# Kernel tuning notes

Measured on AMD Instinct MI355X. Metric: run time of the kernel, lower is better.

The kernel has to match this reference:

```python
import jax, jax.numpy as jnp
import numpy as np

B, S, E, H, V, L = 64, 128, 512, 1024, 32000, 1


def setup_inputs() -> dict:
    key = jax.random.key(0)
    ks = jax.random.split(key, 12)
    def rn(k, shape, scale=0.02):
        return jax.random.normal(k, shape, dtype=jnp.float32) * scale
    return dict(
        emb=rn(ks[0], (B, E), 1.0),
        hidden=rn(ks[1], (L, B, H), 1.0),
        encoder_outputs=rn(ks[2], (S, B, H), 1.0),
        z=rn(ks[3], (B, H), 1.0),
        # Attn('concat'): W_a [H, 2H], bias, scoring vector v [H]
        Wa=rn(ks[4], (H, 2 * H)), ba=jnp.zeros((H,), jnp.float32),
        v=rn(ks[5], (H,)),
        # CustomGRUCell: input/hidden/context/latent-z to 3*H gate projections
        Wx=rn(ks[6], (3 * H, E)), bx=jnp.zeros((3 * H,), jnp.float32),
        Wh=rn(ks[7], (3 * H, H)), bh=jnp.zeros((3 * H,), jnp.float32),
        Wc=rn(ks[8], (3 * H, H)), bc=jnp.zeros((3 * H,), jnp.float32),
        Wz=rn(ks[9], (3 * H, H)), bz=jnp.zeros((3 * H,), jnp.float32),
        # rnn2out: Linear(H, V)
        Wout=rn(ks[10], (V, H)), bout=jnp.zeros((V,), jnp.float32),
    )


def reference(emb, hidden, encoder_outputs, z, Wa, ba, v,
              Wx, bx, Wh, bh, Wc, bc, Wz, bz, Wout, bout):
    h_last = hidden[-1]                                              # [B,H]
    # Bahdanau 'concat' attention: score = v . tanh(Wa @ [h; enc] + ba)
    hS = jnp.broadcast_to(h_last[None], encoder_outputs.shape)       # [S,B,H]
    energy = jnp.tanh(jnp.concatenate([hS, encoder_outputs], axis=-1) @ Wa.T + ba)  # [S,B,H]
    scores = jnp.einsum('sbh,h->bs', energy, v)                      # [B,S]
    attn_weights = jax.nn.softmax(scores, axis=-1)[:, None, :]       # [B,1,S]
    enc_bt = jnp.transpose(encoder_outputs, (1, 0, 2))               # [B,S,H]
    context = jnp.einsum('bos,bsh->bh', attn_weights, enc_bt)        # [B,H]
    # Custom GRU cell: gates get extra context and latent-z additive terms
    gx = emb @ Wx.T + bx                                             # [B,3H]
    gh = h_last @ Wh.T + bh
    gc = context @ Wc.T + bc
    gz = z @ Wz.T + bz
    xr, xu, xn = jnp.split(gx + gc + gz, 3, axis=-1)
    hr, hu, hn = jnp.split(gh, 3, axis=-1)
    r = jax.nn.sigmoid(xr + hr)                                      # reset gate
    u = jax.nn.sigmoid(xu + hu)                                      # update gate
    n = jnp.tanh(xn + r * hn)                                        # candidate
    h_new = (1.0 - u) * n + u * h_last                               # [B,H]
    out = h_new @ Wout.T + bout                                      # [B,V] logits
    return out, h_new[None], attn_weights
```

## Files before the change

kernel.cpp:

```cpp
#include <hip/hip_runtime.h>
#include <hip/hip_bf16.h>
#include <math.h>

#define B_  64
#define S_  128
#define E_  512
#define H_  1024
#define V_  32000
#define H3_ 3072
#define NT_ 16

typedef __attribute__((ext_vector_type(8))) short bf16x8;
typedef __attribute__((ext_vector_type(4))) float f32x4;

__device__ __forceinline__ unsigned short f2b(float f) {
    unsigned int u = __builtin_bit_cast(unsigned int, f);
    u = (u + 0x7fffu + ((u >> 16) & 1u)) >> 16;
    return (unsigned short)u;
}

__global__ void cast_bf16(const float* __restrict__ in, unsigned short* __restrict__ out) {
    const size_t i8 = ((size_t)blockIdx.x * 256 + threadIdx.x) * 8;
    float4 a = *(const float4*)&in[i8];
    float4 b = *(const float4*)&in[i8 + 4];
    unsigned short o[8] = { f2b(a.x), f2b(a.y), f2b(a.z), f2b(a.w),
                            f2b(b.x), f2b(b.y), f2b(b.z), f2b(b.w) };
    *(uint4*)&out[i8] = *(uint4*)o;
}

__global__ void cast_wa2(const float* __restrict__ Wa, unsigned short* __restrict__ out) {
    const int id = blockIdx.x * 256 + threadIdx.x;
    const int n = id >> 7;
    const int kk = (id & 127) * 8;
    const float* src = &Wa[(size_t)n * (2 * H_) + H_ + kk];
    float4 a = *(const float4*)src;
    float4 b = *(const float4*)(src + 4);
    unsigned short o[8] = { f2b(a.x), f2b(a.y), f2b(a.z), f2b(a.w),
                            f2b(b.x), f2b(b.y), f2b(b.z), f2b(b.w) };
    *(uint4*)&out[(size_t)n * H_ + kk] = *(uint4*)o;
}

__device__ __forceinline__ void tile_acc(const float* __restrict__ A, int lda,
                                         const float* __restrict__ Wrow0, int ldw,
                                         int kspan, int t, float c[4][4],
                                         float (*As)[64], float (*Ws)[64]) {
    const int tx = t & 15, ty = t >> 4;
    const int lm = t >> 2;
    const int lk = (t & 3) * 4;
    for (int k0 = 0; k0 < kspan; k0 += 16) {
        float4 av = *(const float4*)&A[lm * lda + k0 + lk];
        float4 wv = *(const float4*)&Wrow0[(size_t)lm * ldw + k0 + lk];
        As[lk + 0][lm] = av.x; As[lk + 1][lm] = av.y;
        As[lk + 2][lm] = av.z; As[lk + 3][lm] = av.w;
        Ws[lk + 0][lm] = wv.x; Ws[lk + 1][lm] = wv.y;
        Ws[lk + 2][lm] = wv.z; Ws[lk + 3][lm] = wv.w;
        __syncthreads();
        #pragma unroll
        for (int k = 0; k < 16; ++k) {
            float4 a = *(const float4*)&As[k][ty * 4];
            float4 w = *(const float4*)&Ws[k][tx * 4];
            c[0][0] += a.x * w.x; c[0][1] += a.x * w.y; c[0][2] += a.x * w.z; c[0][3] += a.x * w.w;
            c[1][0] += a.y * w.x; c[1][1] += a.y * w.y; c[1][2] += a.y * w.z; c[1][3] += a.y * w.w;
            c[2][0] += a.z * w.x; c[2][1] += a.z * w.y; c[2][2] += a.z * w.z; c[2][3] += a.z * w.w;
            c[3][0] += a.w * w.x; c[3][1] += a.w * w.y; c[3][2] += a.w * w.z; c[3][3] += a.w * w.w;
        }
        __syncthreads();
    }
}

__global__ void gemm_nt(const float* __restrict__ A, const float* __restrict__ W,
                        const float* __restrict__ bias, float* __restrict__ C,
                        int N, int K) {
    __shared__ float As[16][64];
    __shared__ float Ws[16][64];
    const int n0 = blockIdx.x * 64;
    const int t  = threadIdx.x;
    const int tx = t & 15, ty = t >> 4;
    float c[4][4];
    #pragma unroll
    for (int i = 0; i < 4; ++i)
        #pragma unroll
        for (int j = 0; j < 4; ++j) c[i][j] = 0.f;
    tile_acc(A, K, &W[(size_t)n0 * K], K, K, t, c, As, Ws);
    #pragma unroll
    for (int i = 0; i < 4; ++i) {
        const int m = ty * 4 + i;
        #pragma unroll
        for (int j = 0; j < 4; ++j) {
            const int n = n0 + tx * 4 + j;
            C[m * N + n] = c[i][j] + bias[n];
        }
    }
}

__global__ __launch_bounds__(256) void wout_mfma(
    const unsigned short* __restrict__ Ab, const float* __restrict__ W,
    const float* __restrict__ bias, float* __restrict__ C) {
    __shared__ unsigned short As[64 * 64];
    __shared__ unsigned short Bs[64 * 64];
    const int n0 = blockIdx.x * 64;
    const int t = threadIdx.x;
    const int lane = t & 63, w = t >> 6;
    const int wr = w >> 1, wc = w & 1;

    f32x4 acc[2][2];
    #pragma unroll
    for (int i = 0; i < 2; ++i)
        #pragma unroll
        for (int j = 0; j < 2; ++j) acc[i][j] = (f32x4){0.f, 0.f, 0.f, 0.f};

    for (int k0 = 0; k0 < H_; k0 += 64) {
        #pragma unroll
        for (int r = 0; r < 2; ++r) {
            const int c = r * 256 + t;
            const int row = c >> 3, slot = c & 7;
            const int sw = slot ^ (row & 7);
            uint4 da = *(const uint4*)&Ab[(size_t)row * H_ + k0 + slot * 8];
            *(uint4*)((char*)As + row * 128 + sw * 16) = da;
        }
        #pragma unroll
        for (int r = 0; r < 4; ++r) {
            const int c = r * 256 + t;
            const int row = c >> 4, q4 = c & 15;
            const float4 wv = *(const float4*)&W[(size_t)(n0 + row) * H_ + k0 + q4 * 4];
            uint2 pk;
            pk.x = (unsigned int)f2b(wv.x) | ((unsigned int)f2b(wv.y) << 16);
            pk.y = (unsigned int)f2b(wv.z) | ((unsigned int)f2b(wv.w) << 16);
            const int slot = q4 >> 1, half = q4 & 1;
            const int sw = slot ^ (row & 7);
            *(uint2*)((char*)Bs + row * 128 + sw * 16 + half * 8) = pk;
        }
        __syncthreads();
        #pragma unroll
        for (int kk = 0; kk < 2; ++kk) {
            bf16x8 a[2], b[2];
            #pragma unroll
            for (int i = 0; i < 2; ++i) {
                const int row = wr * 32 + i * 16 + (lane & 15);
                const int sw = (kk * 4 + (lane >> 4)) ^ (row & 7);
                a[i] = *(const bf16x8*)((const char*)As + row * 128 + sw * 16);
            }
            #pragma unroll
            for (int j = 0; j < 2; ++j) {
                const int row = wc * 32 + j * 16 + (lane & 15);
                const int sw = (kk * 4 + (lane >> 4)) ^ (row & 7);
                b[j] = *(const bf16x8*)((const char*)Bs + row * 128 + sw * 16);
            }
            #pragma unroll
            for (int i = 0; i < 2; ++i)
                #pragma unroll
                for (int j = 0; j < 2; ++j)
                    acc[i][j] = __builtin_amdgcn_mfma_f32_16x16x32_bf16(a[i], b[j], acc[i][j], 0, 0, 0);
        }
        __syncthreads();
    }

    #pragma unroll
    for (int i = 0; i < 2; ++i)
        #pragma unroll
        for (int j = 0; j < 2; ++j) {
            const int n = n0 + wc * 32 + j * 16 + (lane & 15);
            const float bn = bias[n];
            #pragma unroll
            for (int q = 0; q < 4; ++q) {
                const int m = wr * 32 + i * 16 + (lane >> 4) * 4 + q;
                C[(size_t)m * V_ + n] = acc[i][j][q] + bn;
            }
        }
}

__global__ void hproj_splitk(const float* __restrict__ h, const float* __restrict__ Wa,
                             float* __restrict__ hpp) {
    __shared__ float As[16][64];
    __shared__ float Ws[16][64];
    const int n0 = blockIdx.x * 64;
    const int kb = blockIdx.y * 128;
    const int t  = threadIdx.x;
    const int tx = t & 15, ty = t >> 4;
    float c[4][4];
    #pragma unroll
    for (int i = 0; i < 4; ++i)
        #pragma unroll
        for (int j = 0; j < 4; ++j) c[i][j] = 0.f;
    tile_acc(&h[kb], H_, &Wa[(size_t)n0 * (2 * H_) + kb], 2 * H_, 128, t, c, As, Ws);
    float* dst = hpp + (size_t)blockIdx.y * B_ * H_;
    #pragma unroll
    for (int i = 0; i < 4; ++i) {
        const int m = ty * 4 + i;
        #pragma unroll
        for (int j = 0; j < 4; ++j)
            dst[m * H_ + n0 + tx * 4 + j] = c[i][j];
    }
}

__global__ void reduce_hproj(const float* __restrict__ hpp, const float* __restrict__ ba,
                             float* __restrict__ hproj) {
    const int idx = blockIdx.x * 256 + threadIdx.x;
    const int hh = idx & 1023;
    float s = ba[hh];
    #pragma unroll
    for (int c = 0; c < 8; ++c) s += hpp[(size_t)c * B_ * H_ + idx];
    hproj[idx] = s;
}

__global__ void gates_splitk(const float* __restrict__ emb, const float* __restrict__ z,
                             const float* __restrict__ ctx, const float* __restrict__ h,
                             const float* __restrict__ Wx, const float* __restrict__ Wz,
                             const float* __restrict__ Wc, const float* __restrict__ Wh,
                             float* __restrict__ P) {
    __shared__ float As[16][64];
    __shared__ float Ws[16][64];
    const int n0 = blockIdx.x * 64;
    const int yc = blockIdx.y;
    const int t  = threadIdx.x;
    const int tx = t & 15, ty = t >> 4;

    const float* A; const float* W; int lda, kb;
    if (yc == 0)      { A = emb; W = Wx; lda = E_; kb = 0; }
    else if (yc <= 2) { A = z;   W = Wz; lda = H_; kb = (yc - 1) * 512; }
    else if (yc <= 4) { A = ctx; W = Wc; lda = H_; kb = (yc - 3) * 512; }
    else              { A = h;   W = Wh; lda = H_; kb = (yc - 5) * 512; }

    float c[4][4];
    #pragma unroll
    for (int i = 0; i < 4; ++i)
        #pragma unroll
        for (int j = 0; j < 4; ++j) c[i][j] = 0.f;
    tile_acc(&A[kb], lda, &W[(size_t)n0 * lda + kb], lda, 512, t, c, As, Ws);
    float* dst = P + (size_t)yc * B_ * H3_;
    #pragma unroll
    for (int i = 0; i < 4; ++i) {
        const int m = ty * 4 + i;
        #pragma unroll
        for (int j = 0; j < 4; ++j)
            dst[m * H3_ + n0 + tx * 4 + j] = c[i][j];
    }
}

__global__ __launch_bounds__(256) void energy_mfma(
    const unsigned short* __restrict__ Ab, const unsigned short* __restrict__ Bb,
    const float* __restrict__ hproj, const float* __restrict__ v,
    float* __restrict__ partials) {
    __shared__ unsigned short As[128 * 32];
    __shared__ unsigned short Bs[128 * 32];
    const int nb = blockIdx.x;
    const int mb = blockIdx.y;
    const int m0 = mb * 128, n0 = nb * 128;
    const int t = threadIdx.x;
    const int lane = t & 63, w = t >> 6;
    const int wr = w >> 1, wc = w & 1;

    f32x4 acc[4][4];
    #pragma unroll
    for (int i = 0; i < 4; ++i)
        #pragma unroll
        for (int j = 0; j < 4; ++j) acc[i][j] = (f32x4){0.f, 0.f, 0.f, 0.f};

    for (int k0 = 0; k0 < H_; k0 += 32) {
        #pragma unroll
        for (int r = 0; r < 2; ++r) {
            const int c = r * 256 + t;
            const int row = c >> 2, slot = c & 3;
            const int sw = slot ^ ((row >> 1) & 3);
            uint4 da = *(const uint4*)&Ab[(size_t)(m0 + row) * H_ + k0 + slot * 8];
            *(uint4*)((char*)As + row * 64 + sw * 16) = da;
            uint4 db = *(const uint4*)&Bb[(size_t)(n0 + row) * H_ + k0 + slot * 8];
            *(uint4*)((char*)Bs + row * 64 + sw * 16) = db;
        }
        __syncthreads();
        bf16x8 a[4], b[4];
        #pragma unroll
        for (int i = 0; i < 4; ++i) {
            const int row = wr * 64 + i * 16 + (lane & 15);
            const int sw = (lane >> 4) ^ ((row >> 1) & 3);
            a[i] = *(const bf16x8*)((const char*)As + row * 64 + sw * 16);
        }
        #pragma unroll
        for (int j = 0; j < 4; ++j) {
            const int row = wc * 64 + j * 16 + (lane & 15);
            const int sw = (lane >> 4) ^ ((row >> 1) & 3);
            b[j] = *(const bf16x8*)((const char*)Bs + row * 64 + sw * 16);
        }
        #pragma unroll
        for (int i = 0; i < 4; ++i)
            #pragma unroll
            for (int j = 0; j < 4; ++j)
                acc[i][j] = __builtin_amdgcn_mfma_f32_16x16x32_bf16(a[i], b[j], acc[i][j], 0, 0, 0);
        __syncthreads();
    }

    float vj[4];
    #pragma unroll
    for (int j = 0; j < 4; ++j) vj[j] = v[n0 + wc * 64 + j * 16 + (lane & 15)];

    const int s = mb * 2 + wr;
    #pragma unroll
    for (int i = 0; i < 4; ++i) {
        #pragma unroll
        for (int q = 0; q < 4; ++q) {
            const int b = i * 16 + (lane >> 4) * 4 + q;
            float sum = 0.f;
            #pragma unroll
            for (int j = 0; j < 4; ++j) {
                const int n = n0 + wc * 64 + j * 16 + (lane & 15);
                sum += vj[j] * tanhf(acc[i][j][q] + hproj[b * H_ + n]);
            }
            sum += __shfl_xor(sum, 1);
            sum += __shfl_xor(sum, 2);
            sum += __shfl_xor(sum, 4);
            sum += __shfl_xor(sum, 8);
            if ((lane & 15) == 0)
                partials[((size_t)b * S_ + s) * NT_ + nb * 2 + wc] = sum;
        }
    }
}

__global__ void energy_scores(const float* __restrict__ enc, const float* __restrict__ Wa,
                              const float* __restrict__ hproj, const float* __restrict__ v,
                              float* __restrict__ partials) {
    __shared__ float As[16][64];
    __shared__ float Ws[16][64];
    __shared__ float red[64][16];
    const int nt = blockIdx.x;
    const int s  = blockIdx.y;
    const int n0 = nt * 64;
    const float* Arow = enc + (size_t)s * (B_ * H_);
    const int t  = threadIdx.x;
    const int tx = t & 15, ty = t >> 4;
    float c[4][4];
    #pragma unroll
    for (int i = 0; i < 4; ++i)
        #pragma unroll
        for (int j = 0; j < 4; ++j) c[i][j] = 0.f;
    tile_acc(Arow, H_, &Wa[(size_t)n0 * (2 * H_) + H_], 2 * H_, H_, t, c, As, Ws);
    #pragma unroll
    for (int i = 0; i < 4; ++i) {
        const int b = ty * 4 + i;
        float part = 0.f;
        #pragma unroll
        for (int j = 0; j < 4; ++j) {
            const int h = n0 + tx * 4 + j;
            part += v[h] * tanhf(c[i][j] + hproj[b * H_ + h]);
        }
        red[b][tx] = part;
    }
    __syncthreads();
    if (t < 64) {
        float sum = 0.f;
        #pragma unroll
        for (int x = 0; x < 16; ++x) sum += red[t][x];
        partials[((size_t)t * S_ + s) * NT_ + nt] = sum;
    }
}

__global__ void softmax_attn(const float* __restrict__ partials, float* __restrict__ attn_out) {
    __shared__ float red[128];
    const int b = blockIdx.x;
    const int s = threadIdx.x;
    float sc = 0.f;
    #pragma unroll
    for (int nt = 0; nt < NT_; ++nt) sc += partials[((size_t)b * S_ + s) * NT_ + nt];
    red[s] = sc; __syncthreads();
    for (int o = 64; o > 0; o >>= 1) {
        if (s < o) red[s] = fmaxf(red[s], red[s + o]);
        __syncthreads();
    }
    const float mx = red[0]; __syncthreads();
    const float e = expf(sc - mx);
    red[s] = e; __syncthreads();
    for (int o = 64; o > 0; o >>= 1) {
        if (s < o) red[s] += red[s + o];
        __syncthreads();
    }
    attn_out[b * S_ + s] = e / red[0];
}

__global__ void context_k(const float* __restrict__ attn, const float* __restrict__ enc,
                          float* __restrict__ ctx) {
    __shared__ float aw[S_];
    const int b = blockIdx.y;
    const int h = blockIdx.x * 256 + threadIdx.x;
    if (threadIdx.x < S_) aw[threadIdx.x] = attn[b * S_ + threadIdx.x];
    __syncthreads();
    float acc = 0.f;
    for (int s = 0; s < S_; ++s)
        acc += aw[s] * enc[((size_t)s * B_ + b) * H_ + h];
    ctx[b * H_ + h] = acc;
}

__global__ void gru_k(const float* __restrict__ P, const float* __restrict__ hlast,
                      const float* __restrict__ bx, const float* __restrict__ bz,
                      const float* __restrict__ bc, const float* __restrict__ bh,
                      float* __restrict__ hnew) {
    const int idx = blockIdx.x * 256 + threadIdx.x;
    const int b = idx >> 10, h = idx & 1023;
    float x[3], hg[3];
    #pragma unroll
    for (int g = 0; g < 3; ++g) {
        const int col = g * H_ + h;
        float sx = bx[col] + bz[col] + bc[col];
        #pragma unroll
        for (int c = 0; c < 5; ++c) sx += P[((size_t)c * B_ + b) * H3_ + col];
        float sh = bh[col];
        #pragma unroll
        for (int c = 5; c < 7; ++c) sh += P[((size_t)c * B_ + b) * H3_ + col];
        x[g] = sx; hg[g] = sh;
    }
    const float r = 1.f / (1.f + expf(-(x[0] + hg[0])));
    const float u = 1.f / (1.f + expf(-(x[1] + hg[1])));
    const float n = tanhf(x[2] + r * hg[2]);
    hnew[idx] = (1.f - u) * n + u * hlast[idx];
}

extern "C" void kernel_launch(void* const* d_in, const int* in_sizes, int n_in,
                              void* d_out, int out_size, void* d_ws, size_t ws_size,
                              hipStream_t stream) {
    const float* emb   = (const float*)d_in[0];
    const float* hid   = (const float*)d_in[1];
    const float* enc   = (const float*)d_in[2];
    const float* z     = (const float*)d_in[3];
    const float* Wa    = (const float*)d_in[4];
    const float* ba    = (const float*)d_in[5];
    const float* v     = (const float*)d_in[6];
    const float* Wx    = (const float*)d_in[7];
    const float* bx    = (const float*)d_in[8];
    const float* Wh    = (const float*)d_in[9];
    const float* bh    = (const float*)d_in[10];
    const float* Wc    = (const float*)d_in[11];
    const float* bc    = (const float*)d_in[12];
    const float* Wz    = (const float*)d_in[13];
    const float* bz    = (const float*)d_in[14];
    const float* Wout  = (const float*)d_in[15];
    const float* bout  = (const float*)d_in[16];

    float* out  = (float*)d_out;
    float* hnew = out + (size_t)B_ * V_;
    float* attn = hnew + (size_t)B_ * H_;

    float* hproj = (float*)d_ws;
    float* spart = hproj + (size_t)B_ * H_;
    float* ctx   = spart + (size_t)B_ * S_ * NT_;
    float* uni   = ctx + (size_t)B_ * H_;
    unsigned short* encb = (unsigned short*)uni;
    unsigned short* wa2b = encb + (size_t)S_ * B_ * H_;
    float* hpp   = uni;
    float* P     = uni;
    unsigned short* hnewb = (unsigned short*)(P + (size_t)7 * B_ * H3_);
    const size_t need = (size_t)((char*)(wa2b + (size_t)H_ * H_) - (char*)d_ws);

    const float* hlast = hid;
    dim3 blk(256);

    hproj_splitk<<<dim3(H_ / 64, 8), blk, 0, stream>>>(hlast, Wa, hpp);
    reduce_hproj<<<dim3((B_ * H_) / 256), blk, 0, stream>>>(hpp, ba, hproj);

    const bool fast = (ws_size >= need);
    if (fast) {
        cast_bf16<<<dim3((S_ * B_ * H_) / (256 * 8)), blk, 0, stream>>>(enc, encb);
        cast_wa2<<<dim3((H_ * H_) / (256 * 8)), blk, 0, stream>>>(Wa, wa2b);
        energy_mfma<<<dim3(H_ / 128, (S_ * B_) / 128), blk, 0, stream>>>(encb, wa2b, hproj, v, spart);
    } else {
        energy_scores<<<dim3(NT_, S_), blk, 0, stream>>>(enc, Wa, hproj, v, spart);
    }

    softmax_attn<<<dim3(B_), dim3(S_), 0, stream>>>(spart, attn);
    context_k<<<dim3(H_ / 256, B_), blk, 0, stream>>>(attn, enc, ctx);

    gates_splitk<<<dim3(H3_ / 64, 7), blk, 0, stream>>>(emb, z, ctx, hlast,
                                                        Wx, Wz, Wc, Wh, P);
    gru_k<<<dim3((B_ * H_) / 256), blk, 0, stream>>>(P, hlast, bx, bz, bc, bh, hnew);

    if (fast) {
        cast_bf16<<<dim3((B_ * H_) / (256 * 8)), blk, 0, stream>>>(hnew, hnewb);
        wout_mfma<<<dim3(V_ / 64), blk, 0, stream>>>(hnewb, Wout, bout, out);
    } else {
        gemm_nt<<<dim3(V_ / 64), blk, 0, stream>>>(hnew, Wout, bout, out, V_, H_);
    }
}
```

Before: 147.6 us.

## Fuse prologue casts with hproj, merge softmax into context, cast hnew in GRU

The enc and Wa bf16 casts and the hproj split-K GEMM are merged into one heterogeneous prologue launch, so hpp gets its own workspace region instead of aliasing the cast buffers. Softmax is folded into the context kernel, with each block recomputing its batch row's softmax, and the GRU kernel writes the bf16 copy of h_new directly. This removes four launches and lets the small hproj GEMM overlap the bandwidth-bound casts. The cost is redundant softmax work across the four H-blocks per batch and a larger workspace requirement.

```diff
diff --git a/kernel.cpp b/kernel.cpp
--- a/kernel.cpp
+++ b/kernel.cpp
@@ -17,27 +17,6 @@
     unsigned int u = __builtin_bit_cast(unsigned int, f);
     u = (u + 0x7fffu + ((u >> 16) & 1u)) >> 16;
     return (unsigned short)u;
-}
-
-__global__ void cast_bf16(const float* __restrict__ in, unsigned short* __restrict__ out) {
-    const size_t i8 = ((size_t)blockIdx.x * 256 + threadIdx.x) * 8;
-    float4 a = *(const float4*)&in[i8];
-    float4 b = *(const float4*)&in[i8 + 4];
-    unsigned short o[8] = { f2b(a.x), f2b(a.y), f2b(a.z), f2b(a.w),
-                            f2b(b.x), f2b(b.y), f2b(b.z), f2b(b.w) };
-    *(uint4*)&out[i8] = *(uint4*)o;
-}
-
-__global__ void cast_wa2(const float* __restrict__ Wa, unsigned short* __restrict__ out) {
-    const int id = blockIdx.x * 256 + threadIdx.x;
-    const int n = id >> 7;
-    const int kk = (id & 127) * 8;
-    const float* src = &Wa[(size_t)n * (2 * H_) + H_ + kk];
-    float4 a = *(const float4*)src;
-    float4 b = *(const float4*)(src + 4);
-    unsigned short o[8] = { f2b(a.x), f2b(a.y), f2b(a.z), f2b(a.w),
-                            f2b(b.x), f2b(b.y), f2b(b.z), f2b(b.w) };
-    *(uint4*)&out[(size_t)n * H_ + kk] = *(uint4*)o;
 }
 
 __device__ __forceinline__ void tile_acc(const float* __restrict__ A, int lda,
@@ -68,129 +47,64 @@
     }
 }
 
-__global__ void gemm_nt(const float* __restrict__ A, const float* __restrict__ W,
-                        const float* __restrict__ bias, float* __restrict__ C,
-                        int N, int K) {
+__device__ __forceinline__ void hproj_body(int bx, int by, const float* __restrict__ h,
+                                           const float* __restrict__ Wa, float* __restrict__ hpp,
+                                           int t, float (*As)[64], float (*Ws)[64]) {
+    const int n0 = bx * 64;
+    const int kb = by * 128;
+    const int tx = t & 15, ty = t >> 4;
+    float c[4][4];
+    #pragma unroll
+    for (int i = 0; i < 4; ++i)
+        #pragma unroll
+        for (int j = 0; j < 4; ++j) c[i][j] = 0.f;
+    tile_acc(&h[kb], H_, &Wa[(size_t)n0 * (2 * H_) + kb], 2 * H_, 128, t, c, As, Ws);
+    float* dst = hpp + (size_t)by * B_ * H_;
+    #pragma unroll
+    for (int i = 0; i < 4; ++i) {
+        const int m = ty * 4 + i;
+        #pragma unroll
+        for (int j = 0; j < 4; ++j)
+            dst[m * H_ + n0 + tx * 4 + j] = c[i][j];
+    }
+}
+
+__global__ __launch_bounds__(256) void prologue(
+    const float* __restrict__ enc, const float* __restrict__ Wa,
+    const float* __restrict__ h, unsigned short* __restrict__ encb,
+    unsigned short* __restrict__ wa2b, float* __restrict__ hpp) {
     __shared__ float As[16][64];
     __shared__ float Ws[16][64];
-    const int n0 = blockIdx.x * 64;
-    const int t  = threadIdx.x;
-    const int tx = t & 15, ty = t >> 4;
-    float c[4][4];
-    #pragma unroll
-    for (int i = 0; i < 4; ++i)
-        #pragma unroll
-        for (int j = 0; j < 4; ++j) c[i][j] = 0.f;
-    tile_acc(A, K, &W[(size_t)n0 * K], K, K, t, c, As, Ws);
-    #pragma unroll
-    for (int i = 0; i < 4; ++i) {
-        const int m = ty * 4 + i;
-        #pragma unroll
-        for (int j = 0; j < 4; ++j) {
-            const int n = n0 + tx * 4 + j;
-            C[m * N + n] = c[i][j] + bias[n];
-        }
-    }
-}
-
-__global__ __launch_bounds__(256) void wout_mfma(
-    const unsigned short* __restrict__ Ab, const float* __restrict__ W,
-    const float* __restrict__ bias, float* __restrict__ C) {
-    __shared__ unsigned short As[64 * 64];
-    __shared__ unsigned short Bs[64 * 64];
-    const int n0 = blockIdx.x * 64;
+    const int bid = blockIdx.x;
     const int t = threadIdx.x;
-    const int lane = t & 63, w = t >> 6;
-    const int wr = w >> 1, wc = w & 1;
-
-    f32x4 acc[2][2];
-    #pragma unroll
-    for (int i = 0; i < 2; ++i)
-        #pragma unroll
-        for (int j = 0; j < 2; ++j) acc[i][j] = (f32x4){0.f, 0.f, 0.f, 0.f};
-
-    for (int k0 = 0; k0 < H_; k0 += 64) {
-        #pragma unroll
-        for (int r = 0; r < 2; ++r) {
-            const int c = r * 256 + t;
-            const int row = c >> 3, slot = c & 7;
-            const int sw = slot ^ (row & 7);
-            uint4 da = *(const uint4*)&Ab[(size_t)row * H_ + k0 + slot * 8];
-            *(uint4*)((char*)As + row * 128 + sw * 16) = da;
-        }
-        #pragma unroll
-        for (int r = 0; r < 4; ++r) {
-            const int c = r * 256 + t;
-            const int row = c >> 4, q4 = c & 15;
-            const float4 wv = *(const float4*)&W[(size_t)(n0 + row) * H_ + k0 + q4 * 4];
-            uint2 pk;
-            pk.x = (unsigned int)f2b(wv.x) | ((unsigned int)f2b(wv.y) << 16);
-            pk.y = (unsigned int)f2b(wv.z) | ((unsigned int)f2b(wv.w) << 16);
-            const int slot = q4 >> 1, half = q4 & 1;
-            const int sw = slot ^ (row & 7);
-            *(uint2*)((char*)Bs + row * 128 + sw * 16 + half * 8) = pk;
-        }
-        __syncthreads();
-        #pragma unroll
-        for (int kk = 0; kk < 2; ++kk) {
-            bf16x8 a[2], b[2];
-            #pragma unroll
-            for (int i = 0; i < 2; ++i) {
-                const int row = wr * 32 + i * 16 + (lane & 15);
-                const int sw = (kk * 4 + (lane >> 4)) ^ (row & 7);
-                a[i] = *(const bf16x8*)((const char*)As + row * 128 + sw * 16);
-            }
-            #pragma unroll
-            for (int j = 0; j < 2; ++j) {
-                const int row = wc * 32 + j * 16 + (lane & 15);
-                const int sw = (kk * 4 + (lane >> 4)) ^ (row & 7);
-                b[j] = *(const bf16x8*)((const char*)Bs + row * 128 + sw * 16);
-            }
-            #pragma unroll
-            for (int i = 0; i < 2; ++i)
-                #pragma unroll
-                for (int j = 0; j < 2; ++j)
-                    acc[i][j] = __builtin_amdgcn_mfma_f32_16x16x32_bf16(a[i], b[j], acc[i][j], 0, 0, 0);
-        }
-        __syncthreads();
-    }
-
-    #pragma unroll
-    for (int i = 0; i < 2; ++i)
-        #pragma unroll
-        for (int j = 0; j < 2; ++j) {
-            const int n = n0 + wc * 32 + j * 16 + (lane & 15);
-            const float bn = bias[n];
-            #pragma unroll
-            for (int q = 0; q < 4; ++q) {
-                const int m = wr * 32 + i * 16 + (lane >> 4) * 4 + q;
-                C[(size_t)m * V_ + n] = acc[i][j][q] + bn;
-            }
-        }
+    if (bid < 4096) {
+        const size_t i8 = ((size_t)bid * 256 + t) * 8;
+        float4 a = *(const float4*)&enc[i8];
+        float4 b = *(const float4*)&enc[i8 + 4];
+        unsigned short o[8] = { f2b(a.x), f2b(a.y), f2b(a.z), f2b(a.w),
+                                f2b(b.x), f2b(b.y), f2b(b.z), f2b(b.w) };
+        *(uint4*)&encb[i8] = *(uint4*)o;
+    } else if (bid < 4608) {
+        const int id = (bid - 4096) * 256 + t;
+        const int n = id >> 7;
+        const int kk = (id & 127) * 8;
+        const float* src = &Wa[(size_t)n * (2 * H_) + H_ + kk];
+        float4 a = *(const float4*)src;
+        float4 b = *(const float4*)(src + 4);
+        unsigned short o[8] = { f2b(a.x), f2b(a.y), f2b(a.z), f2b(a.w),
+                                f2b(b.x), f2b(b.y), f2b(b.z), f2b(b.w) };
+        *(uint4*)&wa2b[(size_t)n * H_ + kk] = *(uint4*)o;
+    } else {
+        const int id = bid - 4608;
+        hproj_body(id & 15, id >> 4, h, Wa, hpp, t, As, Ws);
+    }
 }
 
 __global__ void hproj_splitk(const float* __restrict__ h, const float* __restrict__ Wa,
                              float* __restrict__ hpp) {
     __shared__ float As[16][64];
     __shared__ float Ws[16][64];
-    const int n0 = blockIdx.x * 64;
-    const int kb = blockIdx.y * 128;
-    const int t  = threadIdx.x;
-    const int tx = t & 15, ty = t >> 4;
-    float c[4][4];
-    #pragma unroll
-    for (int i = 0; i < 4; ++i)
-        #pragma unroll
-        for (int j = 0; j < 4; ++j) c[i][j] = 0.f;
-    tile_acc(&h[kb], H_, &Wa[(size_t)n0 * (2 * H_) + kb], 2 * H_, 128, t, c, As, Ws);
-    float* dst = hpp + (size_t)blockIdx.y * B_ * H_;
-    #pragma unroll
-    for (int i = 0; i < 4; ++i) {
-        const int m = ty * 4 + i;
-        #pragma unroll
-        for (int j = 0; j < 4; ++j)
-            dst[m * H_ + n0 + tx * 4 + j] = c[i][j];
-    }
+    hproj_body(blockIdx.x, blockIdx.y, h, Wa, hpp, threadIdx.x, As, Ws);
 }
 
 __global__ void reduce_hproj(const float* __restrict__ hpp, const float* __restrict__ ba,
@@ -201,40 +115,6 @@
     #pragma unroll
     for (int c = 0; c < 8; ++c) s += hpp[(size_t)c * B_ * H_ + idx];
     hproj[idx] = s;
-}
-
-__global__ void gates_splitk(const float* __restrict__ emb, const float* __restrict__ z,
-                             const float* __restrict__ ctx, const float* __restrict__ h,
-                             const float* __restrict__ Wx, const float* __restrict__ Wz,
-                             const float* __restrict__ Wc, const float* __restrict__ Wh,
-                             float* __restrict__ P) {
-    __shared__ float As[16][64];
-    __shared__ float Ws[16][64];
-    const int n0 = blockIdx.x * 64;
-    const int yc = blockIdx.y;
-    const int t  = threadIdx.x;
-    const int tx = t & 15, ty = t >> 4;
-
-    const float* A; const float* W; int lda, kb;
-    if (yc == 0)      { A = emb; W = Wx; lda = E_; kb = 0; }
-    else if (yc <= 2) { A = z;   W = Wz; lda = H_; kb = (yc - 1) * 512; }
-    else if (yc <= 4) { A = ctx; W = Wc; lda = H_; kb = (yc - 3) * 512; }
-    else              { A = h;   W = Wh; lda = H_; kb = (yc - 5) * 512; }
-
-    float c[4][4];
-    #pragma unroll
-    for (int i = 0; i < 4; ++i)
-        #pragma unroll
-        for (int j = 0; j < 4; ++j) c[i][j] = 0.f;
-    tile_acc(&A[kb], lda, &W[(size_t)n0 * lda + kb], lda, 512, t, c, As, Ws);
-    float* dst = P + (size_t)yc * B_ * H3_;
-    #pragma unroll
-    for (int i = 0; i < 4; ++i) {
-        const int m = ty * 4 + i;
-        #pragma unroll
-        for (int j = 0; j < 4; ++j)
-            dst[m * H3_ + n0 + tx * 4 + j] = c[i][j];
-    }
 }
 
 __global__ __launch_bounds__(256) void energy_mfma(
@@ -353,45 +233,84 @@
     }
 }
 
-__global__ void softmax_attn(const float* __restrict__ partials, float* __restrict__ attn_out) {
+__global__ __launch_bounds__(256) void softmax_ctx(
+    const float* __restrict__ spart, const float* __restrict__ enc,
+    float* __restrict__ attn, float* __restrict__ ctx) {
     __shared__ float red[128];
-    const int b = blockIdx.x;
-    const int s = threadIdx.x;
-    float sc = 0.f;
-    #pragma unroll
-    for (int nt = 0; nt < NT_; ++nt) sc += partials[((size_t)b * S_ + s) * NT_ + nt];
-    red[s] = sc; __syncthreads();
+    __shared__ float aw[128];
+    const int b = blockIdx.y;
+    const int t = threadIdx.x;
+    if (t < 128) {
+        float sc = 0.f;
+        #pragma unroll
+        for (int nt = 0; nt < NT_; ++nt) sc += spart[((size_t)b * S_ + t) * NT_ + nt];
+        aw[t] = sc;
+        red[t] = sc;
+    }
+    __syncthreads();
     for (int o = 64; o > 0; o >>= 1) {
-        if (s < o) red[s] = fmaxf(red[s], red[s + o]);
-        __syncthreads();
-    }
-    const float mx = red[0]; __syncthreads();
-    const float e = expf(sc - mx);
-    red[s] = e; __syncthreads();
+        if (t < o) red[t] = fmaxf(red[t], red[t + o]);
+        __syncthreads();
+    }
+    const float mx = red[0];
+    __syncthreads();
+    if (t < 128) { aw[t] = expf(aw[t] - mx); red[t] = aw[t]; }
+    __syncthreads();
     for (int o = 64; o > 0; o >>= 1) {
-        if (s < o) red[s] += red[s + o];
-        __syncthreads();
-    }
-    attn_out[b * S_ + s] = e / red[0];
-}
-
-__global__ void context_k(const float* __restrict__ attn, const float* __restrict__ enc,
-                          float* __restrict__ ctx) {
-    __shared__ float aw[S_];
-    const int b = blockIdx.y;
-    const int h = blockIdx.x * 256 + threadIdx.x;
-    if (threadIdx.x < S_) aw[threadIdx.x] = attn[b * S_ + threadIdx.x];
+        if (t < o) red[t] += red[t + o];
+        __syncthreads();
+    }
+    const float inv = 1.f / red[0];
+    if (t < 128) {
+        aw[t] *= inv;
+        if (blockIdx.x == 0) attn[b * S_ + t] = aw[t];
+    }
     __syncthreads();
+    const int h = blockIdx.x * 256 + t;
     float acc = 0.f;
     for (int s = 0; s < S_; ++s)
         acc += aw[s] * enc[((size_t)s * B_ + b) * H_ + h];
     ctx[b * H_ + h] = acc;
 }
 
+__global__ void gates_splitk(const float* __restrict__ emb, const float* __restrict__ z,
+                             const float* __restrict__ ctx, const float* __restrict__ h,
+                             const float* __restrict__ Wx, const float* __restrict__ Wz,
+                             const float* __restrict__ Wc, const float* __restrict__ Wh,
+                             float* __restrict__ P) {
+    __shared__ float As[16][64];
+    __shared__ float Ws[16][64];
+    const int n0 = blockIdx.x * 64;
+    const int yc = blockIdx.y;
+    const int t  = threadIdx.x;
+    const int tx = t & 15, ty = t >> 4;
+
+    const float* A; const float* W; int lda, kb;
+    if (yc == 0)      { A = emb; W = Wx; lda = E_; kb = 0; }
+    else if (yc <= 2) { A = z;   W = Wz; lda = H_; kb = (yc - 1) * 512; }
+    else if (yc <= 4) { A = ctx; W = Wc; lda = H_; kb = (yc - 3) * 512; }
+    else              { A = h;   W = Wh; lda = H_; kb = (yc - 5) * 512; }
+
+    float c[4][4];
+    #pragma unroll
+    for (int i = 0; i < 4; ++i)
+        #pragma unroll
+        for (int j = 0; j < 4; ++j) c[i][j] = 0.f;
+    tile_acc(&A[kb], lda, &W[(size_t)n0 * lda + kb], lda, 512, t, c, As, Ws);
+    float* dst = P + (size_t)yc * B_ * H3_;
+    #pragma unroll
+    for (int i = 0; i < 4; ++i) {
+        const int m = ty * 4 + i;
+        #pragma unroll
+        for (int j = 0; j < 4; ++j)
+            dst[m * H3_ + n0 + tx * 4 + j] = c[i][j];
+    }
+}
+
 __global__ void gru_k(const float* __restrict__ P, const float* __restrict__ hlast,
                       const float* __restrict__ bx, const float* __restrict__ bz,
                       const float* __restrict__ bc, const float* __restrict__ bh,
-                      float* __restrict__ hnew) {
+                      float* __restrict__ hnew, unsigned short* __restrict__ hnewb) {
     const int idx = blockIdx.x * 256 + threadIdx.x;
     const int b = idx >> 10, h = idx & 1023;
     float x[3], hg[3];
@@ -409,7 +328,110 @@
     const float r = 1.f / (1.f + expf(-(x[0] + hg[0])));
     const float u = 1.f / (1.f + expf(-(x[1] + hg[1])));
     const float n = tanhf(x[2] + r * hg[2]);
-    hnew[idx] = (1.f - u) * n + u * hlast[idx];
+    const float val = (1.f - u) * n + u * hlast[idx];
+    hnew[idx] = val;
+    if (hnewb) hnewb[idx] = f2b(val);
+}
+
+__global__ __launch_bounds__(256) void wout_mfma(
+    const unsigned short* __restrict__ Ab, const float* __restrict__ W,
+    const float* __restrict__ bias, float* __restrict__ C) {
+    __shared__ unsigned short As[64 * 64];
+    __shared__ unsigned short Bs[64 * 64];
+    const int n0 = blockIdx.x * 64;
+    const int t = threadIdx.x;
+    const int lane = t & 63, w = t >> 6;
+    const int wr = w >> 1, wc = w & 1;
+
+    f32x4 acc[2][2];
+    #pragma unroll
+    for (int i = 0; i < 2; ++i)
+        #pragma unroll
+        for (int j = 0; j < 2; ++j) acc[i][j] = (f32x4){0.f, 0.f, 0.f, 0.f};
+
+    for (int k0 = 0; k0 < H_; k0 += 64) {
+        #pragma unroll
+        for (int r = 0; r < 2; ++r) {
+            const int c = r * 256 + t;
+            const int row = c >> 3, slot = c & 7;
+            const int sw = slot ^ (row & 7);
+            uint4 da = *(const uint4*)&Ab[(size_t)row * H_ + k0 + slot * 8];
+            *(uint4*)((char*)As + row * 128 + sw * 16) = da;
+        }
+        #pragma unroll
+        for (int r = 0; r < 4; ++r) {
+            const int c = r * 256 + t;
+            const int row = c >> 4, q4 = c & 15;
+            const float4 wv = *(const float4*)&W[(size_t)(n0 + row) * H_ + k0 + q4 * 4];
+            uint2 pk;
+            pk.x = (unsigned int)f2b(wv.x) | ((unsigned int)f2b(wv.y) << 16);
+            pk.y = (unsigned int)f2b(wv.z) | ((unsigned int)f2b(wv.w) << 16);
+            const int slot = q4 >> 1, half = q4 & 1;
+            const int sw = slot ^ (row & 7);
+            *(uint2*)((char*)Bs + row * 128 + sw * 16 + half * 8) = pk;
+        }
+        __syncthreads();
+        #pragma unroll
+        for (int kk = 0; kk < 2; ++kk) {
+            bf16x8 a[2], b[2];
+            #pragma unroll
+            for (int i = 0; i < 2; ++i) {
+                const int row = wr * 32 + i * 16 + (lane & 15);
+                const int sw = (kk * 4 + (lane >> 4)) ^ (row & 7);
+                a[i] = *(const bf16x8*)((const char*)As + row * 128 + sw * 16);
+            }
+            #pragma unroll
+            for (int j = 0; j < 2; ++j) {
+                const int row = wc * 32 + j * 16 + (lane & 15);
+                const int sw = (kk * 4 + (lane >> 4)) ^ (row & 7);
+                b[j] = *(const bf16x8*)((const char*)Bs + row * 128 + sw * 16);
+            }
+            #pragma unroll
+            for (int i = 0; i < 2; ++i)
+                #pragma unroll
+                for (int j = 0; j < 2; ++j)
+                    acc[i][j] = __builtin_amdgcn_mfma_f32_16x16x32_bf16(a[i], b[j], acc[i][j], 0, 0, 0);
+        }
+        __syncthreads();
+    }
+
+    #pragma unroll
+    for (int i = 0; i < 2; ++i)
+        #pragma unroll
+        for (int j = 0; j < 2; ++j) {
+            const int n = n0 + wc * 32 + j * 16 + (lane & 15);
+            const float bn = bias[n];
+            #pragma unroll
+            for (int q = 0; q < 4; ++q) {
+                const int m = wr * 32 + i * 16 + (lane >> 4) * 4 + q;
+                C[(size_t)m * V_ + n] = acc[i][j][q] + bn;
+            }
+        }
+}
+
+__global__ void gemm_nt(const float* __restrict__ A, const float* __restrict__ W,
+                        const float* __restrict__ bias, float* __restrict__ C,
+                        int N, int K) {
+    __shared__ float As[16][64];
+    __shared__ float Ws[16][64];
+    const int n0 = blockIdx.x * 64;
+    const int t  = threadIdx.x;
+    const int tx = t & 15, ty = t >> 4;
+    float c[4][4];
+    #pragma unroll
+    for (int i = 0; i < 4; ++i)
+        #pragma unroll
+        for (int j = 0; j < 4; ++j) c[i][j] = 0.f;
+    tile_acc(A, K, &W[(size_t)n0 * K], K, K, t, c, As, Ws);
+    #pragma unroll
+    for (int i = 0; i < 4; ++i) {
+        const int m = ty * 4 + i;
+        #pragma unroll
+        for (int j = 0; j < 4; ++j) {
+            const int n = n0 + tx * 4 + j;
+            C[m * N + n] = c[i][j] + bias[n];
+        }
+    }
 }
 
 extern "C" void kernel_launch(void* const* d_in, const int* in_sizes, int n_in,
@@ -440,38 +462,36 @@
     float* hproj = (float*)d_ws;
     float* spart = hproj + (size_t)B_ * H_;
     float* ctx   = spart + (size_t)B_ * S_ * NT_;
-    float* uni   = ctx + (size_t)B_ * H_;
+    float* hpp   = ctx + (size_t)B_ * H_;
+    float* uni   = hpp + (size_t)8 * B_ * H_;
     unsigned short* encb = (unsigned short*)uni;
     unsigned short* wa2b = encb + (size_t)S_ * B_ * H_;
-    float* hpp   = uni;
-    float* P     = uni;
+    float* P = uni;
     unsigned short* hnewb = (unsigned short*)(P + (size_t)7 * B_ * H3_);
     const size_t need = (size_t)((char*)(wa2b + (size_t)H_ * H_) - (char*)d_ws);
 
     const float* hlast = hid;
     dim3 blk(256);
 
-    hproj_splitk<<<dim3(H_ / 64, 8), blk, 0, stream>>>(hlast, Wa, hpp);
-    reduce_hproj<<<dim3((B_ * H_) / 256), blk, 0, stream>>>(hpp, ba, hproj);
-
     const bool fast = (ws_size >= need);
     if (fast) {
-        cast_bf16<<<dim3((S_ * B_ * H_) / (256 * 8)), blk, 0, stream>>>(enc, encb);
-        cast_wa2<<<dim3((H_ * H_) / (256 * 8)), blk, 0, stream>>>(Wa, wa2b);
+        prologue<<<dim3(4736), blk, 0, stream>>>(enc, Wa, hlast, encb, wa2b, hpp);
+        reduce_hproj<<<dim3((B_ * H_) / 256), blk, 0, stream>>>(hpp, ba, hproj);
         energy_mfma<<<dim3(H_ / 128, (S_ * B_) / 128), blk, 0, stream>>>(encb, wa2b, hproj, v, spart);
     } else {
+        hproj_splitk<<<dim3(H_ / 64, 8), blk, 0, stream>>>(hlast, Wa, hpp);
+        reduce_hproj<<<dim3((B_ * H_) / 256), blk, 0, stream>>>(hpp, ba, hproj);
         energy_scores<<<dim3(NT_, S_), blk, 0, stream>>>(enc, Wa, hproj, v, spart);
     }
 
-    softmax_attn<<<dim3(B_), dim3(S_), 0, stream>>>(spart, attn);
-    context_k<<<dim3(H_ / 256, B_), blk, 0, stream>>>(attn, enc, ctx);
+    softmax_ctx<<<dim3(H_ / 256, B_), blk, 0, stream>>>(spart, enc, attn, ctx);
 
     gates_splitk<<<dim3(H3_ / 64, 7), blk, 0, stream>>>(emb, z, ctx, hlast,
                                                         Wx, Wz, Wc, Wh, P);
-    gru_k<<<dim3((B_ * H_) / 256), blk, 0, stream>>>(P, hlast, bx, bz, bc, bh, hnew);
+    gru_k<<<dim3((B_ * H_) / 256), blk, 0, stream>>>(P, hlast, bx, bz, bc, bh,
+                                                     hnew, fast ? hnewb : nullptr);
 
     if (fast) {
-        cast_bf16<<<dim3((B_ * H_) / (256 * 8)), blk, 0, stream>>>(hnew, hnewb);
         wout_mfma<<<dim3(V_ / 64), blk, 0, stream>>>(hnewb, Wout, bout, out);
     } else {
         gemm_nt<<<dim3(V_ / 64), blk, 0, stream>>>(hnew, Wout, bout, out, V_, H_);
```

New measurement: 142.0 us. 3.8% less time.
